# Optimization experiments

Measured on AMD Instinct MI355X. Metric: run time of the kernel, lower is better.

The kernel has to match this reference:

```python
import jax, jax.numpy as jnp
import numpy as np

F = 200      # number of independent feature MLPs
D_IN = 3
H = 15       # enc_out // 2
ENC = 30     # enc_out
B = 32768


def setup_inputs() -> dict:
    key = jax.random.key(0)
    ky, k1, kb1, k2, kb2, k3, kb3 = jax.random.split(key, 7)
    y = jax.random.normal(ky, (B, F, D_IN), dtype=jnp.float32)
    # Per-feature MLP params, stacked along feature axis (grouped GEMM form).
    W1 = jax.random.normal(k1, (F, D_IN, H), dtype=jnp.float32) * (1.0 / np.sqrt(D_IN))
    b1 = jax.random.normal(kb1, (F, H), dtype=jnp.float32) * 0.01
    W2 = jax.random.normal(k2, (F, H, ENC), dtype=jnp.float32) * (1.0 / np.sqrt(H))
    b2 = jax.random.normal(kb2, (F, ENC), dtype=jnp.float32) * 0.01
    # Final linear over the concatenated [F*ENC] vector.
    W3 = jax.random.normal(k3, (F * ENC, 1), dtype=jnp.float32) * (1.0 / np.sqrt(F * ENC))
    b3 = jax.random.normal(kb3, (1,), dtype=jnp.float32) * 0.01
    return {"y": y, "W1": W1, "b1": b1, "W2": W2, "b2": b2, "W3": W3, "b3": b3}


def reference(y, W1, b1, W2, b2, W3, b3):
    # 200 independent tiny MLPs -> one batched einsum per layer.
    h = jax.nn.relu(jnp.einsum('bfi,fih->bfh', y, W1) + b1)      # [B, F, H]
    h = jax.nn.relu(jnp.einsum('bfh,fhe->bfe', h, W2) + b2)      # [B, F, ENC]
    # torch.cat(res, 1) with res[i] = block_i(y[:, i, :]) == reshape [B, F*ENC]
    flat = h.reshape(h.shape[0], F * ENC)
    return flat @ W3 + b3                                         # [B, 1]
```

## Files before the change

### kernel.cpp

```cpp
#include <hip/hip_runtime.h>
#include <hip/hip_bf16.h>

#define NF  200
#define DIN 3
#define NH  15
#define NE  30
#define NB  32768

typedef __attribute__((ext_vector_type(8)))  short short8;
typedef __attribute__((ext_vector_type(16))) float f32x16;

constexpr int FSPLIT = 25;
constexpr int FPW    = NF / FSPLIT;
constexpr int PAIRS  = FPW / 2;
constexpr int BT     = 256;
constexpr int RPW    = 32;
constexpr int RPB    = 4 * RPW;

constexpr size_t OFF_A1P = 0;
constexpr size_t OFF_W2Q = 102400;
constexpr size_t OFF_W3F = 307200;

__device__ __forceinline__ unsigned f2bfu(float x) {
    __hip_bfloat16 h = __float2bfloat16(x);
    unsigned short u; __builtin_memcpy(&u, &h, 2); return (unsigned)u;
}

__device__ __forceinline__ unsigned cvtpk(float lo, float hi) {
    unsigned r;
    asm("v_cvt_pk_bf16_f32 %0, %1, %2" : "=v"(r) : "v"(lo), "v"(hi));
    return r;
}

__device__ __forceinline__ float2 pkfma(float2 a, float2 b, float2 c) {
    float2 d;
    asm("v_pk_fma_f32 %0, %1, %2, %3" : "=v"(d) : "v"(a), "v"(b), "v"(c));
    return d;
}

__global__ void nn_init(float* __restrict__ out, const float* __restrict__ b3) {
    int i = blockIdx.x * 256 + threadIdx.x;
    if (i < NB) out[i] = b3[0];
}

__global__ void nn_prep(const float* __restrict__ W1, const float* __restrict__ b1,
                        const float* __restrict__ W2, const float* __restrict__ b2,
                        const float* __restrict__ W3, char* __restrict__ ws) {
    const int f = blockIdx.x;
    const int t = threadIdx.x;
    const int x = t & 31, hi = t >> 5;
    unsigned short* A1p = (unsigned short*)(ws + OFF_A1P);
    unsigned short* W2q = (unsigned short*)(ws + OFF_W2Q);
    float*          w3f = (float*)(ws + OFF_W3F);

    {
        unsigned short* d = W2q + ((size_t)f * 64 + t) * 8;
#pragma unroll
        for (int j = 0; j < 8; ++j) {
            const int h = (j & 3) + 8 * (j >> 2) + 4 * hi;
            float v = 0.f;
            if (x < NE) v = (h < NH) ? W2[((size_t)f * NH + h) * NE + x]
                                     : b2[f * NE + x];
            d[j] = (unsigned short)f2bfu(v);
        }
    }
    if (t < 32) {
        const int hh = t >> 4, r = t & 15;
        const int e = (r & 3) + 8 * (r >> 2) + 4 * hh;
        w3f[(size_t)f * 32 + t] = (e < NE) ? W3[f * NE + e] : 0.f;
    }

    if ((f & 1) == 0) {
        unsigned short* a = A1p + ((size_t)(f >> 1) * 64 + t) * 8;
#pragma unroll
        for (int j = 0; j < 8; ++j) {
            float v = 0.f;
            if (hi == 0) {
                if (x < 16) {
                    if (x < NH) {
                        if (j < 3)       v = W1[((size_t)f * DIN + j) * NH + x];
                        else if (j == 3) v = b1[f * NH + x];
                    }
                } else {
                    const int h = x - 16;
                    if (h < NH) {
                        if (j >= 4 && j < 7) v = W1[((size_t)(f + 1) * DIN + (j - 4)) * NH + h];
                        else if (j == 7)     v = b1[(f + 1) * NH + h];
                    }
                }
            }
            a[j] = (unsigned short)f2bfu(v);
        }
    }
}

__global__ __launch_bounds__(BT, 5)
void nn_main(const float* __restrict__ y, const char* __restrict__ ws,
             float* __restrict__ out) {
    __shared__ __align__(16) short sA1[PAIRS * 512];
    __shared__ __align__(16) short sW2[FPW * 512];
    __shared__ __align__(16) float sW3f[FPW * 32];

    const int t  = threadIdx.x;
    const int w  = t >> 6;
    const int l  = t & 63;
    const int ln = l & 31;
    const int hi = l >> 5;
    const int r0 = blockIdx.x * RPB + w * RPW;
    const int f0 = blockIdx.y * FPW;
    const int p0 = f0 >> 1;

    const float4* __restrict__ yp4 = reinterpret_cast<const float4*>(
        y + (size_t)(r0 + ln) * (NF * DIN) + (size_t)f0 * DIN);
    const float4 c0 = yp4[0], c1 = yp4[1], c2 = yp4[2];
    const float4 c3 = yp4[3], c4 = yp4[4], c5 = yp4[5];

    {
        const uint4* gA = (const uint4*)(ws + OFF_A1P + (size_t)p0 * 1024);
        const uint4* gW = (const uint4*)(ws + OFF_W2Q + (size_t)f0 * 1024);
        const uint4* g3 = (const uint4*)(ws + OFF_W3F + (size_t)f0 * 128);
        uint4* dA = (uint4*)sA1;
        uint4* dW = (uint4*)sW2;
        uint4* d3 = (uint4*)sW3f;
        dA[t] = gA[t];
        dW[t]       = gW[t];
        dW[t + 256] = gW[t + 256];
        if (t < 64) d3[t] = g3[t];
    }
    __syncthreads();

    const short* __restrict__ a1l = sA1 + l * 8;
    const short* __restrict__ w2l = sW2 + l * 8;

    const unsigned himask = hi ? 0x3F800000u : 0u;
    const float onef = 1.0f;
    const f32x16 zc = {};

    float2 acc0 = {0.f, 0.f};
    float2 acc1 = {0.f, 0.f};

    auto epilogue = [&](const f32x16& d2, const float* __restrict__ wf) {
        float r[16];
#pragma unroll
        for (int i = 0; i < 16; ++i) r[i] = fmaxf(d2[i], 0.f);
        const float4 w0  = ((const float4*)wf)[0];
        const float4 w1  = ((const float4*)wf)[1];
        const float4 w2_ = ((const float4*)wf)[2];
        const float4 w3_ = ((const float4*)wf)[3];
        acc0 = pkfma(float2{r[0],  r[1]},  float2{w0.x,  w0.y},  acc0);
        acc1 = pkfma(float2{r[2],  r[3]},  float2{w0.z,  w0.w},  acc1);
        acc0 = pkfma(float2{r[4],  r[5]},  float2{w1.x,  w1.y},  acc0);
        acc1 = pkfma(float2{r[6],  r[7]},  float2{w1.z,  w1.w},  acc1);
        acc0 = pkfma(float2{r[8],  r[9]},  float2{w2_.x, w2_.y}, acc0);
        acc1 = pkfma(float2{r[10], r[11]}, float2{w2_.z, w2_.w}, acc1);
        acc0 = pkfma(float2{r[12], r[13]}, float2{w3_.x, w3_.y}, acc0);
        acc1 = pkfma(float2{r[14], r[15]}, float2{w3_.z, w3_.w}, acc1);
    };

    auto pair_body = [&](int pp, float y0A, float y1A, float y2A,
                                 float y0B, float y1B, float y2B) {
        const short8 A1  = *reinterpret_cast<const short8*>(a1l + (size_t)pp * 512);
        const short8 W2A = *reinterpret_cast<const short8*>(w2l + (size_t)(2 * pp) * 512);
        const short8 W2B = *reinterpret_cast<const short8*>(w2l + (size_t)(2 * pp + 1) * 512);

        union { unsigned u[4]; short8 s; } B1;
        B1.u[0] = cvtpk(y0A, y1A);
        B1.u[1] = cvtpk(y2A, onef);
        B1.u[2] = cvtpk(y0B, y1B);
        B1.u[3] = cvtpk(y2B, onef);

        const f32x16 d1 = __builtin_amdgcn_mfma_f32_32x32x16_bf16(A1, B1.s, zc, 0, 0, 0);

        union { unsigned u[4]; short8 s; } PA, PB;
#pragma unroll
        for (int i = 0; i < 4; ++i) {
            PA.u[i] = cvtpk(fmaxf(d1[2 * i], 0.f),     fmaxf(d1[2 * i + 1], 0.f));
            PB.u[i] = cvtpk(fmaxf(d1[8 + 2 * i], 0.f), fmaxf(d1[8 + 2 * i + 1], 0.f));
        }
        PA.u[3] |= himask;
        PB.u[3] |= himask;

        const f32x16 dA2 = __builtin_amdgcn_mfma_f32_32x32x16_bf16(W2A, PA.s, zc, 0, 0, 0);
        epilogue(dA2, sW3f + (2 * pp) * 32 + hi * 16);
        const f32x16 dB2 = __builtin_amdgcn_mfma_f32_32x32x16_bf16(W2B, PB.s, zc, 0, 0, 0);
        epilogue(dB2, sW3f + (2 * pp + 1) * 32 + hi * 16);
    };

    pair_body(0, c0.x, c0.y, c0.z,  c0.w, c1.x, c1.y);
    pair_body(1, c1.z, c1.w, c2.x,  c2.y, c2.z, c2.w);
    pair_body(2, c3.x, c3.y, c3.z,  c3.w, c4.x, c4.y);
    pair_body(3, c4.z, c4.w, c5.x,  c5.y, c5.z, c5.w);

    float partial = (acc0.x + acc1.x) + (acc0.y + acc1.y);
    partial += __shfl_xor(partial, 32);
    if (hi == 0) atomicAdd(&out[r0 + ln], partial);
}

extern "C" void kernel_launch(void* const* d_in, const int* in_sizes, int n_in,
                              void* d_out, int out_size, void* d_ws, size_t ws_size,
                              hipStream_t stream) {
    const float* y  = (const float*)d_in[0];
    const float* W1 = (const float*)d_in[1];
    const float* b1 = (const float*)d_in[2];
    const float* W2 = (const float*)d_in[3];
    const float* b2 = (const float*)d_in[4];
    const float* W3 = (const float*)d_in[5];
    const float* b3 = (const float*)d_in[6];
    float* out = (float*)d_out;

    nn_prep<<<dim3(NF), dim3(64), 0, stream>>>(W1, b1, W2, b2, W3, (char*)d_ws);
    nn_init<<<dim3((NB + 255) / 256), dim3(256), 0, stream>>>(out, b3);
    nn_main<<<dim3(NB / RPB, FSPLIT), dim3(BT), 0, stream>>>(
        y, (const char*)d_ws, out);
}
```

Baseline: 42.61 us.

## Process two row tiles per wave to reuse shared-memory weights

Each wave now handles two 32-row tiles (r0 and r0+128), so one block covers 256 rows instead of 128. The weight fragments loaded from LDS and the staging of weights per block are amortized over twice the rows, and the two independent MFMA chains can interleave. The cost is more registers (launch bounds drop from 5 to 4 waves per SIMD), half as many blocks, and y loads split into two phases.

```diff
diff --git a/kernel.cpp b/kernel.cpp
--- a/kernel.cpp
+++ b/kernel.cpp
@@ -14,8 +14,7 @@
 constexpr int FPW    = NF / FSPLIT;
 constexpr int PAIRS  = FPW / 2;
 constexpr int BT     = 256;
-constexpr int RPW    = 32;
-constexpr int RPB    = 4 * RPW;
+constexpr int RPB    = 256;
 
 constexpr size_t OFF_A1P = 0;
 constexpr size_t OFF_W2Q = 102400;
@@ -94,7 +93,7 @@
     }
 }
 
-__global__ __launch_bounds__(BT, 5)
+__global__ __launch_bounds__(BT, 4)
 void nn_main(const float* __restrict__ y, const char* __restrict__ ws,
              float* __restrict__ out) {
     __shared__ __align__(16) short sA1[PAIRS * 512];
@@ -106,14 +105,15 @@
     const int l  = t & 63;
     const int ln = l & 31;
     const int hi = l >> 5;
-    const int r0 = blockIdx.x * RPB + w * RPW;
+    const int r0 = blockIdx.x * RPB + w * 32;
+    const int r1 = r0 + 128;
     const int f0 = blockIdx.y * FPW;
     const int p0 = f0 >> 1;
 
-    const float4* __restrict__ yp4 = reinterpret_cast<const float4*>(
+    const float4* __restrict__ ya4 = reinterpret_cast<const float4*>(
         y + (size_t)(r0 + ln) * (NF * DIN) + (size_t)f0 * DIN);
-    const float4 c0 = yp4[0], c1 = yp4[1], c2 = yp4[2];
-    const float4 c3 = yp4[3], c4 = yp4[4], c5 = yp4[5];
+    const float4* __restrict__ yb4 = reinterpret_cast<const float4*>(
+        y + (size_t)(r1 + ln) * (NF * DIN) + (size_t)f0 * DIN);
 
     {
         const uint4* gA = (const uint4*)(ws + OFF_A1P + (size_t)p0 * 1024);
@@ -136,10 +136,11 @@
     const float onef = 1.0f;
     const f32x16 zc = {};
 
-    float2 acc0 = {0.f, 0.f};
-    float2 acc1 = {0.f, 0.f};
-
-    auto epilogue = [&](const f32x16& d2, const float* __restrict__ wf) {
+    float2 a0t0 = {0.f, 0.f}, a1t0 = {0.f, 0.f};
+    float2 a0t1 = {0.f, 0.f}, a1t1 = {0.f, 0.f};
+
+    auto epi = [&](const f32x16& d2, const float* __restrict__ wf,
+                   float2& e0, float2& e1) {
         float r[16];
 #pragma unroll
         for (int i = 0; i < 16; ++i) r[i] = fmaxf(d2[i], 0.f);
@@ -147,53 +148,81 @@
         const float4 w1  = ((const float4*)wf)[1];
         const float4 w2_ = ((const float4*)wf)[2];
         const float4 w3_ = ((const float4*)wf)[3];
-        acc0 = pkfma(float2{r[0],  r[1]},  float2{w0.x,  w0.y},  acc0);
-        acc1 = pkfma(float2{r[2],  r[3]},  float2{w0.z,  w0.w},  acc1);
-        acc0 = pkfma(float2{r[4],  r[5]},  float2{w1.x,  w1.y},  acc0);
-        acc1 = pkfma(float2{r[6],  r[7]},  float2{w1.z,  w1.w},  acc1);
-        acc0 = pkfma(float2{r[8],  r[9]},  float2{w2_.x, w2_.y}, acc0);
-        acc1 = pkfma(float2{r[10], r[11]}, float2{w2_.z, w2_.w}, acc1);
-        acc0 = pkfma(float2{r[12], r[13]}, float2{w3_.x, w3_.y}, acc0);
-        acc1 = pkfma(float2{r[14], r[15]}, float2{w3_.z, w3_.w}, acc1);
+        e0 = pkfma(float2{r[0],  r[1]},  float2{w0.x,  w0.y},  e0);
+        e1 = pkfma(float2{r[2],  r[3]},  float2{w0.z,  w0.w},  e1);
+        e0 = pkfma(float2{r[4],  r[5]},  float2{w1.x,  w1.y},  e0);
+        e1 = pkfma(float2{r[6],  r[7]},  float2{w1.z,  w1.w},  e1);
+        e0 = pkfma(float2{r[8],  r[9]},  float2{w2_.x, w2_.y}, e0);
+        e1 = pkfma(float2{r[10], r[11]}, float2{w2_.z, w2_.w}, e1);
+        e0 = pkfma(float2{r[12], r[13]}, float2{w3_.x, w3_.y}, e0);
+        e1 = pkfma(float2{r[14], r[15]}, float2{w3_.z, w3_.w}, e1);
     };
 
-    auto pair_body = [&](int pp, float y0A, float y1A, float y2A,
-                                 float y0B, float y1B, float y2B) {
+    auto pair_body = [&](int pp,
+                         float x0A, float x1A, float x2A, float x0B, float x1B, float x2B,
+                         float z0A, float z1A, float z2A, float z0B, float z1B, float z2B) {
         const short8 A1  = *reinterpret_cast<const short8*>(a1l + (size_t)pp * 512);
         const short8 W2A = *reinterpret_cast<const short8*>(w2l + (size_t)(2 * pp) * 512);
         const short8 W2B = *reinterpret_cast<const short8*>(w2l + (size_t)(2 * pp + 1) * 512);
 
-        union { unsigned u[4]; short8 s; } B1;
-        B1.u[0] = cvtpk(y0A, y1A);
-        B1.u[1] = cvtpk(y2A, onef);
-        B1.u[2] = cvtpk(y0B, y1B);
-        B1.u[3] = cvtpk(y2B, onef);
-
-        const f32x16 d1 = __builtin_amdgcn_mfma_f32_32x32x16_bf16(A1, B1.s, zc, 0, 0, 0);
-
-        union { unsigned u[4]; short8 s; } PA, PB;
+        union { unsigned u[4]; short8 s; } B0, B1v;
+        B0.u[0]  = cvtpk(x0A, x1A);  B0.u[1]  = cvtpk(x2A, onef);
+        B0.u[2]  = cvtpk(x0B, x1B);  B0.u[3]  = cvtpk(x2B, onef);
+        B1v.u[0] = cvtpk(z0A, z1A);  B1v.u[1] = cvtpk(z2A, onef);
+        B1v.u[2] = cvtpk(z0B, z1B);  B1v.u[3] = cvtpk(z2B, onef);
+
+        const f32x16 d1_0 = __builtin_amdgcn_mfma_f32_32x32x16_bf16(A1, B0.s,  zc, 0, 0, 0);
+        const f32x16 d1_1 = __builtin_amdgcn_mfma_f32_32x32x16_bf16(A1, B1v.s, zc, 0, 0, 0);
+
+        union { unsigned u[4]; short8 s; } PA0, PB0, PA1, PB1;
 #pragma unroll
         for (int i = 0; i < 4; ++i) {
-            PA.u[i] = cvtpk(fmaxf(d1[2 * i], 0.f),     fmaxf(d1[2 * i + 1], 0.f));
-            PB.u[i] = cvtpk(fmaxf(d1[8 + 2 * i], 0.f), fmaxf(d1[8 + 2 * i + 1], 0.f));
+            PA0.u[i] = cvtpk(fmaxf(d1_0[2 * i], 0.f),     fmaxf(d1_0[2 * i + 1], 0.f));
+            PB0.u[i] = cvtpk(fmaxf(d1_0[8 + 2 * i], 0.f), fmaxf(d1_0[8 + 2 * i + 1], 0.f));
+            PA1.u[i] = cvtpk(fmaxf(d1_1[2 * i], 0.f),     fmaxf(d1_1[2 * i + 1], 0.f));
+            PB1.u[i] = cvtpk(fmaxf(d1_1[8 + 2 * i], 0.f), fmaxf(d1_1[8 + 2 * i + 1], 0.f));
         }
-        PA.u[3] |= himask;
-        PB.u[3] |= himask;
-
-        const f32x16 dA2 = __builtin_amdgcn_mfma_f32_32x32x16_bf16(W2A, PA.s, zc, 0, 0, 0);
-        epilogue(dA2, sW3f + (2 * pp) * 32 + hi * 16);
-        const f32x16 dB2 = __builtin_amdgcn_mfma_f32_32x32x16_bf16(W2B, PB.s, zc, 0, 0, 0);
-        epilogue(dB2, sW3f + (2 * pp + 1) * 32 + hi * 16);
+        PA0.u[3] |= himask;  PB0.u[3] |= himask;
+        PA1.u[3] |= himask;  PB1.u[3] |= himask;
+
+        const float* wfA = sW3f + (2 * pp) * 32 + hi * 16;
+        const float* wfB = sW3f + (2 * pp + 1) * 32 + hi * 16;
+
+        const f32x16 dA0 = __builtin_amdgcn_mfma_f32_32x32x16_bf16(W2A, PA0.s, zc, 0, 0, 0);
+        epi(dA0, wfA, a0t0, a1t0);
+        const f32x16 dA1 = __builtin_amdgcn_mfma_f32_32x32x16_bf16(W2A, PA1.s, zc, 0, 0, 0);
+        epi(dA1, wfA, a0t1, a1t1);
+        const f32x16 dB0 = __builtin_amdgcn_mfma_f32_32x32x16_bf16(W2B, PB0.s, zc, 0, 0, 0);
+        epi(dB0, wfB, a0t0, a1t0);
+        const f32x16 dB1 = __builtin_amdgcn_mfma_f32_32x32x16_bf16(W2B, PB1.s, zc, 0, 0, 0);
+        epi(dB1, wfB, a0t1, a1t1);
     };
 
-    pair_body(0, c0.x, c0.y, c0.z,  c0.w, c1.x, c1.y);
-    pair_body(1, c1.z, c1.w, c2.x,  c2.y, c2.z, c2.w);
-    pair_body(2, c3.x, c3.y, c3.z,  c3.w, c4.x, c4.y);
-    pair_body(3, c4.z, c4.w, c5.x,  c5.y, c5.z, c5.w);
-
-    float partial = (acc0.x + acc1.x) + (acc0.y + acc1.y);
-    partial += __shfl_xor(partial, 32);
-    if (hi == 0) atomicAdd(&out[r0 + ln], partial);
+    {
+        const float4 c0 = ya4[0], c1 = ya4[1], c2 = ya4[2];
+        const float4 d0 = yb4[0], d1 = yb4[1], d2 = yb4[2];
+        pair_body(0, c0.x, c0.y, c0.z,  c0.w, c1.x, c1.y,
+                     d0.x, d0.y, d0.z,  d0.w, d1.x, d1.y);
+        pair_body(1, c1.z, c1.w, c2.x,  c2.y, c2.z, c2.w,
+                     d1.z, d1.w, d2.x,  d2.y, d2.z, d2.w);
+    }
+    {
+        const float4 c0 = ya4[3], c1 = ya4[4], c2 = ya4[5];
+        const float4 d0 = yb4[3], d1 = yb4[4], d2 = yb4[5];
+        pair_body(2, c0.x, c0.y, c0.z,  c0.w, c1.x, c1.y,
+                     d0.x, d0.y, d0.z,  d0.w, d1.x, d1.y);
+        pair_body(3, c1.z, c1.w, c2.x,  c2.y, c2.z, c2.w,
+                     d1.z, d1.w, d2.x,  d2.y, d2.z, d2.w);
+    }
+
+    float p0s = (a0t0.x + a1t0.x) + (a0t0.y + a1t0.y);
+    float p1s = (a0t1.x + a1t1.x) + (a0t1.y + a1t1.y);
+    p0s += __shfl_xor(p0s, 32);
+    p1s += __shfl_xor(p1s, 32);
+    if (hi == 0) {
+        atomicAdd(&out[r0 + ln], p0s);
+        atomicAdd(&out[r1 + ln], p1s);
+    }
 }
 
 extern "C" void kernel_launch(void* const* d_in, const int* in_sizes, int n_in,
```

Measured after the change: 42.91 us. About the same (+0.7%).
